# Kernel optimization log

Hardware: AMD Instinct MI355X
Metric: run time of the kernel (lower is better)

## Reference

```python
import jax, jax.numpy as jnp
import numpy as np

N = 131072
E = 524288
H = 128
EPS = 1e-5

def _layernorm(h, g, b):
    mu = jnp.mean(h, axis=-1, keepdims=True)
    var = jnp.mean((h - mu) ** 2, axis=-1, keepdims=True)
    return (h - mu) * jax.lax.rsqrt(var + EPS) * g + b

def _node_to_node(x, senders, receivers, valid, num_nodes, params):
    # two-way (symmetrized) message passing: gather + scatter_add, then MLP+LN
    W1, b1, W2, b2, W3, b3, g, beta = params
    tws = jnp.concatenate([senders, receivers])
    twr = jnp.concatenate([receivers, senders])
    msg = x[tws]  # [2E', H] gather
    if valid is not None:
        msg = jnp.where(jnp.concatenate([valid, valid])[:, None], msg, 0.0)
    agg = jax.ops.segment_sum(msg, twr, num_segments=num_nodes)  # scatter_add
    h = jax.nn.gelu(agg @ W1 + b1, approximate=False)
    h = jax.nn.gelu(h @ W2 + b2, approximate=False)
    h = h @ W3 + b3
    return _layernorm(h, g, beta)

def setup_inputs() -> dict:
    key = jax.random.key(0)
    ks = jax.random.split(key, 20)
    s = 0.05
    inp = {
        "x": jax.random.normal(ks[0], (N, H), dtype=jnp.float32),
        "edge_index": jax.random.randint(ks[1], (2, E), 0, N, dtype=jnp.int32),
        "pool_p": jax.random.normal(ks[2], (H,), dtype=jnp.float32),
    }
    names = ["dW1", "db1", "dW2", "db2", "dW3", "db3", "dg", "dbeta",
             "uW1", "ub1", "uW2", "ub2", "uW3", "ub3", "ug", "ubeta"]
    shapes = [(H, H), (H,), (H, H), (H,), (H, H), (H,), (H,), (H,),
              (2 * H, H), (H,), (H, H), (H,), (H, H), (H,), (H,), (H,)]
    for i, (nm, sh) in enumerate(zip(names, shapes)):
        if nm in ("dg", "ug"):
            inp[nm] = jnp.ones(sh, dtype=jnp.float32)
        elif nm in ("dbeta", "ubeta") or nm.startswith(("db", "ub")):
            inp[nm] = jnp.zeros(sh, dtype=jnp.float32)
        else:
            inp[nm] = jax.random.normal(ks[3 + i], sh, dtype=jnp.float32) * s
    return inp

def reference(x, edge_index, pool_p,
              dW1, db1, dW2, db2, dW3, db3, dg, dbeta,
              uW1, ub1, uW2, ub2, uW3, ub3, ug, ubeta):
    senders, receivers = edge_index[0], edge_index[1]
    k = N // 2  # TopKPooling ratio=0.5

    # ---- down: TopKPooling ----
    score = x @ pool_p / jnp.linalg.norm(pool_p)  # [N]
    _, perm = jax.lax.top_k(score, k)             # kept node indices
    x_skip = x
    x_p = x[perm] * jnp.tanh(score[perm])[:, None]  # [k, H]
    mask = jnp.zeros((N,), dtype=bool).at[perm].set(True)
    mapping = jnp.zeros((N,), dtype=jnp.int32).at[perm].set(
        jnp.arange(k, dtype=jnp.int32))
    valid = mask[senders] & mask[receivers]
    ps, pr = mapping[senders], mapping[receivers]

    # down conv on pooled graph
    x_d = _node_to_node(x_p, ps, pr, valid, k,
                        (dW1, db1, dW2, db2, dW3, db3, dg, dbeta))

    # ---- up: unpool (indexed scatter write) + skip concat + up conv ----
    recovered = jnp.zeros_like(x_skip).at[perm].set(x_d)
    x_u = jnp.concatenate([recovered, x_skip], axis=-1)  # [N, 2H]
    out = _node_to_node(x_u, senders, receivers, None, N,
                        (uW1, ub1, uW2, ub2, uW3, ub3, ug, ubeta))
    return out
```

## Files before the change

### kernel.cpp

```cpp
#include <hip/hip_runtime.h>

#define N_NODES 131072
#define N_EDGES 524288
#define K_TOP   65536
#define LN_EPS  1e-5f
#define N_TILES (N_NODES / 64)
#define BCAP    5120u

typedef unsigned int u32;
typedef unsigned short u16;
typedef unsigned long long u64;

typedef __attribute__((ext_vector_type(8))) short bf8;
typedef __attribute__((ext_vector_type(4))) float f4;

#define ST_OFF    0
#define CANON_OFF (64u<<10)
#define PART_OFF  (576u<<10)
#define KEYS_OFF  (1u<<20)
#define TVAL_OFF  (2u<<20)
#define KEPT_OFF  ((2u<<20)+(512u<<10))
#define SBUF_OFF  (3u<<20)
#define ADJ_OFF   (35u<<20)


#define C_DW1 0
#define C_DB1 16384
#define C_DW2 16512
#define C_DB2 32896
#define C_DW3 33024
#define C_DB3 49408
#define C_DG  49536
#define C_DBE 49664
#define C_UW1 49792
#define C_UB1 82560
#define C_UW2 82688
#define C_UB2 99072
#define C_UW3 99200
#define C_UB3 115584
#define C_UG  115712
#define C_UBE 115840
#define C_TOT 115968
#define CT_DW1 115968
#define CT_DW2 132352
#define CT_DW3 148736
#define CT_UW1 165120
#define CT_UW2 197888
#define CT_UW3 214272
#define CT_TOT 230656

__device__ __forceinline__ float bflo(u32 u){ return __uint_as_float(u << 16); }
__device__ __forceinline__ float bfhi(u32 u){ return __uint_as_float(u & 0xFFFF0000u); }
__device__ __forceinline__ float bf2f(u16 v){ return __uint_as_float(((u32)v) << 16); }
__device__ __forceinline__ u32 f2bf(float f){
  u32 u = __float_as_uint(f);
  return (u + 0x7FFFu + ((u >> 16) & 1u)) >> 16;
}
__device__ __forceinline__ float gelu_f(float x){
  return 0.5f * x * (1.0f + erff(x * 0.7071067811865476f));
}
__device__ __forceinline__ float2 f2add(float2 a, float2 b){
  return make_float2(a.x + b.x, a.y + b.y);
}

__device__ __forceinline__ int swz16(int row, int cc){
  return row * 128 + ((cc ^ (row & 15)) * 8);
}

__device__ __forceinline__ bf8 ld_bf16_chunk(const u32* __restrict__ rowp, int s, int quad){
  uint4 v = *(const uint4*)(rowp + s * 16 + quad * 4);
  return __builtin_bit_cast(bf8, v);
}
__device__ __forceinline__ bf8 scale_bf16_chunk(const u32* __restrict__ rowp, int s, int quad, float tv){
  uint4 v = *(const uint4*)(rowp + s * 16 + quad * 4);
  uint4 q;
  q.x = f2bf(bflo(v.x) * tv) | (f2bf(bfhi(v.x) * tv) << 16);
  q.y = f2bf(bflo(v.y) * tv) | (f2bf(bfhi(v.y) * tv) << 16);
  q.z = f2bf(bflo(v.z) * tv) | (f2bf(bfhi(v.z) * tv) << 16);
  q.w = f2bf(bflo(v.w) * tv) | (f2bf(bfhi(v.w) * tv) << 16);
  return __builtin_bit_cast(bf8, q);
}
__device__ __forceinline__ bf8 cvt_f32_chunk(const float* __restrict__ rowp, int s, int quad, float tv){
  const float* p = rowp + s * 32 + quad * 8;
  float4 f0 = *(const float4*)p;
  float4 f1 = *(const float4*)(p + 4);
  uint4 q;
  q.x = f2bf(f0.x * tv) | (f2bf(f0.y * tv) << 16);
  q.y = f2bf(f0.z * tv) | (f2bf(f0.w * tv) << 16);
  q.z = f2bf(f1.x * tv) | (f2bf(f1.y * tv) << 16);
  q.w = f2bf(f1.z * tv) | (f2bf(f1.w * tv) << 16);
  return __builtin_bit_cast(bf8, q);
}

__device__ __forceinline__ void gemm_ab(const u16* ws, const bf8 a[4], int mn, int quad, f4 acc[8]){
  #pragma unroll
  for (int s = 0; s < 4; s++){
    #pragma unroll
    for (int j = 0; j < 8; j++){
      bf8 b = *(const bf8*)&ws[swz16(j * 16 + mn, s * 4 + quad)];
      acc[j] = __builtin_amdgcn_mfma_f32_16x16x32_bf16(a[s], b, acc[j], 0, 0, 0);
    }
  }
}

struct SelState {
  u64 prefix;
  u32 krem, eqcnt;
  int is_f32;
  u32 pad;
  double inv_norm;
  u32 eqlist[4096];
  u64 eqkey[4096];
};

struct P16 { const void* q[16]; };

__device__ __forceinline__ void chain_step(const u32* __restrict__ tots, int q,
                                           u32* sfx, u32* selb, int t,
                                           u64& pref, u32& target){
  sfx[t] = tots[q * 256 + t];
  __syncthreads();
  for (int o = 1; o < 256; o <<= 1){
    u32 x = (t + o < 256) ? sfx[t + o] : 0u;
    __syncthreads();
    sfx[t] += x;
    __syncthreads();
  }
  u32 above = (t == 255) ? 0u : sfx[t + 1];
  if (sfx[t] >= target && above < target){ selb[0] = (u32)t; selb[1] = target - above; }
  __syncthreads();
  pref = (pref << 8) | (u64)selb[0];
  target = selb[1];
  __syncthreads();
}

__global__ void k_detect(const u32* __restrict__ xw, SelState* st){
  int t = threadIdx.x;
  int cnt = 0;
  for (int i = t; i < 4096; i += 256){
    u32 w = xw[(size_t)i * 2048];
    u32 e = (w >> 23) & 0xFFu;
    if (e >= 97u && e <= 135u) cnt++;
  }
  __shared__ int sh[256];
  sh[t] = cnt; __syncthreads();
  for (int o = 128; o > 0; o >>= 1){ if (t < o) sh[t] += sh[t+o]; __syncthreads(); }
  if (t == 0){
    st->is_f32 = (sh[0] >= 3072) ? 1 : 0;
    st->prefix = 0; st->krem = K_TOP; st->eqcnt = 0;
  }
}

__global__ void k_canon(P16 ps, const SelState* __restrict__ st, u16* __restrict__ canon,
                        u32* __restrict__ tots, u32* __restrict__ gcur){
  int i = blockIdx.x * 256 + threadIdx.x;
  if (i < 1024) tots[i] = 0u;
  if (i < 256)  gcur[i] = (u32)i * BCAP;
  if (i >= CT_TOT) return;
  int isf = st->is_f32;
  if (i < C_TOT){
    const int off[17] = {C_DW1,C_DB1,C_DW2,C_DB2,C_DW3,C_DB3,C_DG,C_DBE,
                         C_UW1,C_UB1,C_UW2,C_UB2,C_UW3,C_UB3,C_UG,C_UBE,C_TOT};
    int seg = 0;
    #pragma unroll
    for (int s2 = 0; s2 < 16; s2++) if (i >= off[s2+1]) seg = s2 + 1;
    int j = i - off[seg];
    if (isf) canon[i] = (u16)f2bf(((const float*)ps.q[seg])[j]);
    else     canon[i] = ((const u16*)ps.q[seg])[j];
  } else {
    const int dst[7] = {CT_DW1, CT_DW2, CT_DW3, CT_UW1, CT_UW2, CT_UW3, CT_TOT};
    const int wq[6]  = {0, 2, 4, 8, 10, 12};
    int g = i;
    int seg = 0;
    #pragma unroll
    for (int s2 = 0; s2 < 6; s2++) if (g >= dst[s2+1]) seg = s2 + 1;
    int loc = g - dst[seg];
    int K = (seg == 3) ? 256 : 128;
    int n = loc / K, k = loc % K;
    int src = k * 128 + n;
    if (isf) canon[g] = (u16)f2bf(((const float*)ps.q[wq[seg]])[src]);
    else     canon[g] = ((const u16*)ps.q[wq[seg]])[src];
  }
}

__global__ __launch_bounds__(256) void k_score(const void* __restrict__ xraw, const void* __restrict__ praw,
                        const SelState* __restrict__ st,
                        u64* __restrict__ keys, float* __restrict__ tval){
  int t = threadIdx.x, lane = t & 63, w = t >> 6;
  int n = blockIdx.x * 4 + w;
  double d, ps;
  if (st->is_f32){
    const float* xf = (const float*)xraw + (size_t)n * 128;
    const float* pf = (const float*)praw;
    double p0 = (double)pf[lane], p1 = (double)pf[64 + lane];
    d  = (double)xf[lane] * p0 + (double)xf[64 + lane] * p1;
    ps = p0 * p0 + p1 * p1;
  } else {
    const u32* xw = (const u32*)xraw + (size_t)n * 64;
    const u32* pw = (const u32*)praw;
    u32 xx = xw[lane], pv = pw[lane];
    double p0 = (double)bflo(pv), p1 = (double)bfhi(pv);
    d  = (double)bflo(xx) * p0 + (double)bfhi(xx) * p1;
    ps = p0 * p0 + p1 * p1;
  }
  for (int o = 32; o > 0; o >>= 1){
    d  += __shfl_down(d,  o, 64);
    ps += __shfl_down(ps, o, 64);
  }
  if (lane == 0){
    double sc = d * (1.0 / sqrt(ps));
    u64 u = (u64)__double_as_longlong(sc);
    u64 key = (u & 0x8000000000000000ULL) ? ~u : (u | 0x8000000000000000ULL);
    keys[n] = key;
    tval[n] = tanhf((float)sc);
  }
}

__global__ __launch_bounds__(256) void k_histp(const u64* __restrict__ keys,
                                               u32* __restrict__ tots, int pass){
  __shared__ u32 sfx[256];
  __shared__ u32 selb[2];
  __shared__ u32 h[256];
  int t = threadIdx.x;
  u64 pref = 0;
  u32 target = K_TOP;
  for (int q = 0; q < pass; q++)
    chain_step(tots, q, sfx, selb, t, pref, target);
  h[t] = 0;
  __syncthreads();
  int sh_d = 56 - 8 * pass;
  for (int n = blockIdx.x * 256 + t; n < N_NODES; n += 256 * 256){
    u64 k = keys[n];
    bool m = (pass == 0) ? true : ((k >> (sh_d + 8)) == pref);
    if (m) atomicAdd(&h[(u32)((k >> sh_d) & 255)], 1u);
  }
  __syncthreads();
  if (h[t]) atomicAdd(&tots[pass * 256 + t], h[t]);
}

__global__ __launch_bounds__(256) void k_mark(const u64* __restrict__ keys,
                                              const u32* __restrict__ tots,
                                              SelState* st, u32* __restrict__ kept){
  __shared__ u32 sfx[256];
  __shared__ u32 selb[2];
  int t = threadIdx.x;
  u64 pref = 0;
  u32 target = K_TOP;
  for (int q = 0; q < 4; q++)
    chain_step(tots, q, sfx, selb, t, pref, target);
  u32 T = (u32)pref;
  int n = blockIdx.x * 256 + t;
  u64 k = keys[n];
  u32 t32 = (u32)(k >> 32);
  kept[n] = (t32 > T) ? 1u : 0u;
  if (t32 == T){
    u32 i = atomicAdd(&st->eqcnt, 1u);
    if (i < 4096){ st->eqlist[i] = (u32)n; st->eqkey[i] = k; }
  }
}

__global__ __launch_bounds__(256) void k_tie(const u32* __restrict__ tots,
                                             SelState* st, u32* __restrict__ kept){
  __shared__ u32 sfx[256];
  __shared__ u32 selb[2];
  int t = threadIdx.x;
  u64 pref = 0;
  u32 target = K_TOP;
  for (int q = 0; q < 4; q++)
    chain_step(tots, q, sfx, selb, t, pref, target);
  u32 r = target;
  u32 m = st->eqcnt; if (m > 4096) m = 4096;
  for (u32 i = t; i < m; i += 256){
    u64 ki = st->eqkey[i]; u32 ii = st->eqlist[i];
    u32 rank = 0;
    for (u32 j = 0; j < m; j++){
      u64 kj = st->eqkey[j];
      rank += (kj > ki || (kj == ki && st->eqlist[j] < ii)) ? 1u : 0u;
    }
    if (rank < r) kept[ii] = 1u;
  }
}

__global__ __launch_bounds__(256) void k_bin(const int* __restrict__ se, const int* __restrict__ re,
                                             u32* __restrict__ gcur, u32* __restrict__ pairs){
  __shared__ u32 cnt[256], sc[256], base[256], cur[256], gpos[256];
  __shared__ u32 stage[8192];
  int t = threadIdx.x;
  cnt[t] = 0;
  __syncthreads();
  int e0 = blockIdx.x * 4096;
  for (int i = t; i < 4096; i += 256){
    int s = se[e0 + i], r = re[e0 + i];
    atomicAdd(&cnt[(u32)r >> 9], 1u);
    atomicAdd(&cnt[(u32)s >> 9], 1u);
  }
  __syncthreads();
  sc[t] = cnt[t];
  __syncthreads();
  for (int o = 1; o < 256; o <<= 1){
    u32 x = (t >= o) ? sc[t - o] : 0u;
    __syncthreads();
    sc[t] += x;
    __syncthreads();
  }
  base[t] = sc[t] - cnt[t];
  cur[t] = base[t];
  gpos[t] = atomicAdd(&gcur[t], cnt[t]);
  __syncthreads();
  for (int i = t; i < 4096; i += 256){
    u32 s = (u32)se[e0 + i], r = (u32)re[e0 + i];
    u32 b1 = r >> 9, p1 = ((r & 511u) << 17) | s;
    u32 b2 = s >> 9, p2 = ((s & 511u) << 17) | r;
    stage[atomicAdd(&cur[b1], 1u)] = p1;
    stage[atomicAdd(&cur[b2], 1u)] = p2;
  }
  __syncthreads();
  int lane = t & 63, wv = t >> 6;
  for (int b = wv; b < 256; b += 4){
    u32 n = cnt[b], src = base[b], dst = gpos[b];
    for (u32 i = lane; i < n; i += 64)
      pairs[dst + i] = stage[src + i];
  }
}

__global__ __launch_bounds__(256) void k_place(const u32* __restrict__ gcur,
                                               const u32* __restrict__ pairs,
                                               u32* __restrict__ adj,
                                               u32* __restrict__ off, u32* __restrict__ end){
  __shared__ u32 cnt[512], cur[512], lo[512], ex2[256];
  int b = blockIdx.x, t = threadIdx.x;
  u32 base = (u32)b * BCAP;
  u32 total = gcur[b] - base;
  cnt[t] = 0; cnt[t + 256] = 0; cur[t] = 0; cur[t + 256] = 0;
  __syncthreads();
  for (u32 i = t; i < total; i += 256)
    atomicAdd(&cnt[pairs[base + i] >> 17], 1u);
  __syncthreads();
  u32 c0 = cnt[2 * t], c1 = cnt[2 * t + 1];
  ex2[t] = c0 + c1;
  __syncthreads();
  for (int o = 1; o < 256; o <<= 1){
    u32 x = (t >= o) ? ex2[t - o] : 0u;
    __syncthreads();
    ex2[t] += x;
    __syncthreads();
  }
  u32 e0 = ex2[t] - c0 - c1;
  int n0 = b * 512 + 2 * t;
  off[n0]     = base + e0;        end[n0]     = base + e0 + c0;
  off[n0 + 1] = base + e0 + c0;   end[n0 + 1] = base + e0 + c0 + c1;
  lo[2 * t] = e0; lo[2 * t + 1] = e0 + c0;
  __syncthreads();
  for (u32 i = t; i < total; i += 256){
    u32 p = pairs[base + i];
    u32 nl = p >> 17;
    u32 slot = base + lo[nl] + atomicAdd(&cur[nl], 1u);
    adj[slot] = p & 0x1FFFFu;
  }
}


__global__ __launch_bounds__(256, 3) void k_proj_down(
    const void* __restrict__ xraw, const float* __restrict__ tval,
    const u16* __restrict__ W1T, const SelState* __restrict__ st,
    const u32* __restrict__ kept, u32* __restrict__ S)
{
  __shared__ u16 w1s[128 * 128];
  __shared__ u16 os[64 * 128];
  int t = threadIdx.x, lane = t & 63, wv = t >> 6;
  int m0 = wv * 16, mn = lane & 15, quad = lane >> 4;

  for (int i = t; i < 2048; i += 256){
    int row = i >> 4, cc = i & 15;
    *(uint4*)&w1s[swz16(row, cc)] = *(const uint4*)(W1T + row * 128 + cc * 8);
  }
  int isf = st->is_f32;
  __syncthreads();

  for (int tile = blockIdx.x; tile < N_TILES; tile += gridDim.x){
    int row0 = tile * 64;
    int arow = row0 + m0 + mn;
    float tv = tval[arow];
    bf8 a[4];
    if (isf){
      const float* xf = (const float*)xraw + (size_t)arow * 128;
      #pragma unroll
      for (int s = 0; s < 4; s++) a[s] = cvt_f32_chunk(xf, s, quad, tv);
    } else {
      const u32* xw = (const u32*)xraw + (size_t)arow * 64;
      #pragma unroll
      for (int s = 0; s < 4; s++) a[s] = scale_bf16_chunk(xw, s, quad, tv);
    }
    f4 acc[8];
    #pragma unroll
    for (int j = 0; j < 8; j++){ acc[j][0]=0.f; acc[j][1]=0.f; acc[j][2]=0.f; acc[j][3]=0.f; }
    gemm_ab(w1s, a, mn, quad, acc);

    #pragma unroll
    for (int j = 0; j < 8; j++){
      int c = j * 16 + mn;
      #pragma unroll
      for (int rg = 0; rg < 4; rg++){
        int row = m0 + quad * 4 + rg;
        os[row * 128 + ((c >> 3) ^ (row & 15)) * 8 + (c & 7)] = (u16)f2bf(acc[j][rg]);
      }
    }
    __builtin_amdgcn_wave_barrier();
    int rl = m0 + (lane >> 2), qt = lane & 3;
    u32 kp = kept[row0 + rl];
    u32* out = S + (size_t)(row0 + rl) * 64;
    #pragma unroll
    for (int i = 0; i < 4; i++){
      int cc = qt * 4 + i;
      uint4 w = *(const uint4*)&os[swz16(rl, cc)];
      if (!kp){ w.x = 0; w.y = 0; w.z = 0; w.w = 0; }
      *(uint4*)(out + cc * 4) = w;
    }
    __builtin_amdgcn_wave_barrier();
  }
}

__global__ __launch_bounds__(256, 2) void k_proj_up(
    const u32* __restrict__ R, const void* __restrict__ xraw,
    const u16* __restrict__ W1T, const SelState* __restrict__ st,
    u32* __restrict__ S2)
{
  __shared__ u16 was[128 * 128];
  __shared__ u16 wbs[128 * 128];
  __shared__ u16 os[64 * 128];
  int t = threadIdx.x, lane = t & 63, wv = t >> 6;
  int m0 = wv * 16, mn = lane & 15, quad = lane >> 4;

  for (int i = t; i < 2048; i += 256){
    int row = i >> 4, cc = i & 15;
    *(uint4*)&was[swz16(row, cc)] = *(const uint4*)(W1T + row * 256 + cc * 8);
    *(uint4*)&wbs[swz16(row, cc)] = *(const uint4*)(W1T + row * 256 + 128 + cc * 8);
  }
  int isf = st->is_f32;
  __syncthreads();

  for (int tile = blockIdx.x; tile < N_TILES; tile += gridDim.x){
    int row0 = tile * 64;
    int arow = row0 + m0 + mn;
    bf8 a[4];
    const u32* rp = R + (size_t)arow * 64;
    #pragma unroll
    for (int s = 0; s < 4; s++) a[s] = ld_bf16_chunk(rp, s, quad);
    f4 acc[8];
    #pragma unroll
    for (int j = 0; j < 8; j++){ acc[j][0]=0.f; acc[j][1]=0.f; acc[j][2]=0.f; acc[j][3]=0.f; }
    gemm_ab(was, a, mn, quad, acc);

    if (isf){
      const float* xf = (const float*)xraw + (size_t)arow * 128;
      #pragma unroll
      for (int s = 0; s < 4; s++) a[s] = cvt_f32_chunk(xf, s, quad, 1.0f);
    } else {
      const u32* xw = (const u32*)xraw + (size_t)arow * 64;
      #pragma unroll
      for (int s = 0; s < 4; s++) a[s] = ld_bf16_chunk(xw, s, quad);
    }
    gemm_ab(wbs, a, mn, quad, acc);

    #pragma unroll
    for (int j = 0; j < 8; j++){
      int c = j * 16 + mn;
      #pragma unroll
      for (int rg = 0; rg < 4; rg++){
        int row = m0 + quad * 4 + rg;
        os[row * 128 + ((c >> 3) ^ (row & 15)) * 8 + (c & 7)] = (u16)f2bf(acc[j][rg]);
      }
    }
    __builtin_amdgcn_wave_barrier();
    int rl = m0 + (lane >> 2), qt = lane & 3;
    u32* out = S2 + (size_t)(row0 + rl) * 64;
    #pragma unroll
    for (int i = 0; i < 4; i++){
      int cc = qt * 4 + i;
      *(uint4*)(out + cc * 4) = *(const uint4*)&os[swz16(rl, cc)];
    }
    __builtin_amdgcn_wave_barrier();
  }
}

template<int IS_DOWN>
__global__ __launch_bounds__(256, 4) void k_agg(
    const u32* __restrict__ Smsg, const u32* __restrict__ off, const u32* __restrict__ end,
    const u32* __restrict__ adj,
    const u16* __restrict__ cb1, const u32* __restrict__ kept,
    u32* __restrict__ H)
{
  int t = threadIdx.x, lane = t & 63, wv = t >> 6;
  float b1l = bf2f(cb1[2 * lane]), b1h = bf2f(cb1[2 * lane + 1]);
  int base = blockIdx.x * 16 + wv * 4;
  #pragma unroll 1
  for (int rr = 0; rr < 4; rr++){
    int n = base + rr;
    if (IS_DOWN && !kept[n]){ H[(size_t)n * 64 + lane] = 0u; continue; }
    u32 jb = off[n], je = end[n];
    float2 a = make_float2(0.f, 0.f);
    u32 j = jb;
    for (; j + 8 <= je; j += 8){
      u32 e0 = adj[j],   e1 = adj[j+1], e2 = adj[j+2], e3 = adj[j+3];
      u32 e4 = adj[j+4], e5 = adj[j+5], e6 = adj[j+6], e7 = adj[j+7];
      u32 w0 = Smsg[(size_t)e0 * 64 + lane];
      u32 w1 = Smsg[(size_t)e1 * 64 + lane];
      u32 w2 = Smsg[(size_t)e2 * 64 + lane];
      u32 w3 = Smsg[(size_t)e3 * 64 + lane];
      u32 w4 = Smsg[(size_t)e4 * 64 + lane];
      u32 w5 = Smsg[(size_t)e5 * 64 + lane];
      u32 w6 = Smsg[(size_t)e6 * 64 + lane];
      u32 w7 = Smsg[(size_t)e7 * 64 + lane];
      float2 v0 = make_float2(bflo(w0), bfhi(w0));
      float2 v1 = make_float2(bflo(w1), bfhi(w1));
      float2 v2 = make_float2(bflo(w2), bfhi(w2));
      float2 v3 = make_float2(bflo(w3), bfhi(w3));
      float2 v4 = make_float2(bflo(w4), bfhi(w4));
      float2 v5 = make_float2(bflo(w5), bfhi(w5));
      float2 v6 = make_float2(bflo(w6), bfhi(w6));
      float2 v7 = make_float2(bflo(w7), bfhi(w7));
      a = f2add(a, f2add(f2add(f2add(v0, v1), f2add(v2, v3)),
                         f2add(f2add(v4, v5), f2add(v6, v7))));
    }
    for (; j + 4 <= je; j += 4){
      u32 e0 = adj[j], e1 = adj[j+1], e2 = adj[j+2], e3 = adj[j+3];
      u32 w0 = Smsg[(size_t)e0 * 64 + lane];
      u32 w1 = Smsg[(size_t)e1 * 64 + lane];
      u32 w2 = Smsg[(size_t)e2 * 64 + lane];
      u32 w3 = Smsg[(size_t)e3 * 64 + lane];
      float2 v0 = make_float2(bflo(w0), bfhi(w0));
      float2 v1 = make_float2(bflo(w1), bfhi(w1));
      float2 v2 = make_float2(bflo(w2), bfhi(w2));
      float2 v3 = make_float2(bflo(w3), bfhi(w3));
      a = f2add(a, f2add(f2add(v0, v1), f2add(v2, v3)));
    }
    for (; j < je; j++){
      u32 w = Smsg[(size_t)adj[j] * 64 + lane];
      a = f2add(a, make_float2(bflo(w), bfhi(w)));
    }
    H[(size_t)n * 64 + lane] = f2bf(gelu_f(a.x + b1l)) | (f2bf(gelu_f(a.y + b1h)) << 16);
  }
}

template<int IS_DOWN>
__global__ __launch_bounds__(256, 2) void k_mlp(
    const u32* __restrict__ H,
    const u16* __restrict__ cW2T, const u16* __restrict__ cb2,
    const u16* __restrict__ cW3T, const u16* __restrict__ cb3,
    const u16* __restrict__ cg, const u16* __restrict__ cbe,
    const u32* __restrict__ kept, const SelState* __restrict__ st,
    u32* __restrict__ Rout, void* __restrict__ fout)
{
  __shared__ u16 w2s[128 * 128];
  __shared__ u16 w3s[128 * 128];
  __shared__ u16 os[64 * 128];
  int t = threadIdx.x, lane = t & 63, wv = t >> 6;
  int m0 = wv * 16, mn = lane & 15, quad = lane >> 4;

  for (int i = t; i < 2048; i += 256){
    int row = i >> 4, cc = i & 15;
    *(uint4*)&w2s[swz16(row, cc)] = *(const uint4*)(cW2T + row * 128 + cc * 8);
    *(uint4*)&w3s[swz16(row, cc)] = *(const uint4*)(cW3T + row * 128 + cc * 8);
  }
  float b2v[8], b3v[8], gv[8], bev[8];
  #pragma unroll
  for (int j = 0; j < 8; j++){
    int c = j * 16 + mn;
    b2v[j] = bf2f(cb2[c]); b3v[j] = bf2f(cb3[c]);
    gv[j]  = bf2f(cg[c]);  bev[j] = bf2f(cbe[c]);
  }
  int isf = st->is_f32;
  __syncthreads();

  for (int tile = blockIdx.x; tile < N_TILES; tile += gridDim.x){
    int row0 = tile * 64;
    int arow = row0 + m0 + mn;

    bf8 a[4];
    const u32* hp = H + (size_t)arow * 64;
    #pragma unroll
    for (int s = 0; s < 4; s++) a[s] = ld_bf16_chunk(hp, s, quad);
    f4 acc[8];
    #pragma unroll
    for (int j = 0; j < 8; j++){ acc[j][0]=0.f; acc[j][1]=0.f; acc[j][2]=0.f; acc[j][3]=0.f; }
    gemm_ab(w2s, a, mn, quad, acc);

    #pragma unroll
    for (int j = 0; j < 8; j++){
      int c = j * 16 + mn;
      #pragma unroll
      for (int rg = 0; rg < 4; rg++){
        int row = m0 + quad * 4 + rg;
        os[row * 128 + ((c >> 3) ^ (row & 15)) * 8 + (c & 7)] = (u16)f2bf(gelu_f(acc[j][rg] + b2v[j]));
      }
    }
    __builtin_amdgcn_wave_barrier();

    #pragma unroll
    for (int s = 0; s < 4; s++) a[s] = *(const bf8*)&os[swz16(m0 + mn, s * 4 + quad)];
    #pragma unroll
    for (int j = 0; j < 8; j++){ acc[j][0]=0.f; acc[j][1]=0.f; acc[j][2]=0.f; acc[j][3]=0.f; }
    gemm_ab(w3s, a, mn, quad, acc);

    #pragma unroll
    for (int j = 0; j < 8; j++){
      #pragma unroll
      for (int rg = 0; rg < 4; rg++) acc[j][rg] += b3v[j];
    }
    float s1[4] = {0.f,0.f,0.f,0.f}, s2[4] = {0.f,0.f,0.f,0.f};
    #pragma unroll
    for (int j = 0; j < 8; j++){
      #pragma unroll
      for (int rg = 0; rg < 4; rg++){
        float v = acc[j][rg];
        s1[rg] += v; s2[rg] += v * v;
      }
    }
    #pragma unroll
    for (int o = 1; o < 16; o <<= 1){
      #pragma unroll
      for (int rg = 0; rg < 4; rg++){
        s1[rg] += __shfl_xor(s1[rg], o, 64);
        s2[rg] += __shfl_xor(s2[rg], o, 64);
      }
    }
    float mu[4], rs[4];
    #pragma unroll
    for (int rg = 0; rg < 4; rg++){
      mu[rg] = s1[rg] * 0.0078125f;
      float var = s2[rg] * 0.0078125f - mu[rg] * mu[rg];
      rs[rg] = rsqrtf(var + LN_EPS);
    }
    #pragma unroll
    for (int j = 0; j < 8; j++){
      #pragma unroll
      for (int rg = 0; rg < 4; rg++)
        acc[j][rg] = (acc[j][rg] - mu[rg]) * rs[rg] * gv[j] + bev[j];
    }

    if (!IS_DOWN && isf){
      float* fo = (float*)fout;
      #pragma unroll
      for (int j = 0; j < 8; j++){
        #pragma unroll
        for (int rg = 0; rg < 4; rg++)
          fo[(size_t)(row0 + m0 + quad * 4 + rg) * 128 + j * 16 + mn] = acc[j][rg];
      }
      continue;
    }

    __builtin_amdgcn_wave_barrier();
    #pragma unroll
    for (int j = 0; j < 8; j++){
      int c = j * 16 + mn;
      #pragma unroll
      for (int rg = 0; rg < 4; rg++){
        int row = m0 + quad * 4 + rg;
        os[row * 128 + ((c >> 3) ^ (row & 15)) * 8 + (c & 7)] = (u16)f2bf(acc[j][rg]);
      }
    }
    __builtin_amdgcn_wave_barrier();
    int rl = m0 + (lane >> 2), qt = lane & 3;
    u32 kp = IS_DOWN ? kept[row0 + rl] : 1u;
    u32* out = (IS_DOWN ? Rout : (u32*)fout) + (size_t)(row0 + rl) * 64;
    #pragma unroll
    for (int i = 0; i < 4; i++){
      int cc = qt * 4 + i;
      uint4 w = *(const uint4*)&os[swz16(rl, cc)];
      if (!kp){ w.x = 0; w.y = 0; w.z = 0; w.w = 0; }
      *(uint4*)(out + cc * 4) = w;
    }
    __builtin_amdgcn_wave_barrier();
  }
}


extern "C" void kernel_launch(void* const* d_in, const int* in_sizes, int n_in,
                              void* d_out, int out_size, void* d_ws, size_t ws_size,
                              hipStream_t stream)
{
  const void* x     = d_in[0];
  const int* eidx   = (const int*)d_in[1];
  const void* poolp = d_in[2];
  const int* senders = eidx;
  const int* receivers = eidx + N_EDGES;

  char* ws = (char*)d_ws;
  SelState* st = (SelState*)(ws + ST_OFF);
  u16*  canon  = (u16*) (ws + CANON_OFF);
  u32*  tots   = (u32*) (ws + PART_OFF);
  u32*  gcur   = (u32*) (ws + PART_OFF + 4096);
  u64*  keys   = (u64*) (ws + KEYS_OFF);
  u32*  off    = (u32*) (ws + KEYS_OFF);
  u32*  end    = (u32*) (ws + KEYS_OFF + (512u<<10));
  float* tval  = (float*)(ws + TVAL_OFF);
  u32*  kept   = (u32*) (ws + KEPT_OFF);
  u32*  Sbuf   = (u32*) (ws + SBUF_OFF);
  u32*  adj    = (u32*) (ws + ADJ_OFF);
  u32*  pairs  = Sbuf;
  u32*  Dbuf   = (u32*) d_out;

  P16 ps;
  for (int i = 0; i < 16; i++) ps.q[i] = d_in[3 + i];

  k_detect<<<1, 256, 0, stream>>>((const u32*)x, st);
  k_canon<<<(CT_TOT + 255) / 256, 256, 0, stream>>>(ps, st, canon, tots, gcur);
  k_score<<<N_NODES / 4, 256, 0, stream>>>(x, poolp, st, keys, tval);
  for (int pass = 0; pass < 4; pass++)
    k_histp<<<256, 256, 0, stream>>>(keys, tots, pass);
  k_mark<<<N_NODES / 256, 256, 0, stream>>>(keys, tots, st, kept);
  k_tie<<<1, 256, 0, stream>>>(tots, st, kept);

  k_bin<<<N_EDGES / 4096, 256, 0, stream>>>(senders, receivers, gcur, pairs);
  k_place<<<256, 256, 0, stream>>>(gcur, pairs, adj, off, end);

  k_proj_down<<<768, 256, 0, stream>>>(x, tval, canon + CT_DW1, st, kept, Sbuf);
  k_agg<1><<<N_NODES / 16, 256, 0, stream>>>(Sbuf, off, end, adj, canon + C_DB1, kept, Dbuf);
  k_mlp<1><<<512, 256, 0, stream>>>(Dbuf,
      canon + CT_DW2, canon + C_DB2, canon + CT_DW3, canon + C_DB3,
      canon + C_DG, canon + C_DBE, kept, st, Sbuf, nullptr);

  k_proj_up<<<512, 256, 0, stream>>>(Sbuf, x, canon + CT_UW1, st, Dbuf);
  k_agg<0><<<N_NODES / 16, 256, 0, stream>>>(Dbuf, off, end, adj, canon + C_UB1, kept, Sbuf);
  k_mlp<0><<<512, 256, 0, stream>>>(Sbuf,
      canon + CT_UW2, canon + C_UB2, canon + CT_UW3, canon + C_UB3,
      canon + C_UG, canon + C_UBE, kept, st, nullptr, d_out);
}
```

Measured before the change: 449.8 us.

## Partition adjacency by kept neighbours so down aggregation skips dropped nodes

k_place now counts, for each node, how many neighbours are kept and orders each adjacency list with kept neighbours first. It packs the kept count and the total count into one word that replaces the end array. The down-pass aggregation reads only the kept prefix, so it no longer gathers zeroed rows of dropped nodes (about three quarters of neighbours when half the nodes are kept). Because those rows are never read, k_proj_down also stops writing them, which saves memory traffic. The cost is extra kept lookups and atomics in k_place.

```diff
diff --git a/kernel.cpp b/kernel.cpp
--- a/kernel.cpp
+++ b/kernel.cpp
@@ -325,16 +325,24 @@
 
 __global__ __launch_bounds__(256) void k_place(const u32* __restrict__ gcur,
                                                const u32* __restrict__ pairs,
+                                               const u32* __restrict__ kept,
                                                u32* __restrict__ adj,
-                                               u32* __restrict__ off, u32* __restrict__ end){
-  __shared__ u32 cnt[512], cur[512], lo[512], ex2[256];
+                                               u32* __restrict__ off, u32* __restrict__ cnts){
+  __shared__ u32 cnt[512], ck[512], curk[512], curn[512], lo[512], ex2[256];
   int b = blockIdx.x, t = threadIdx.x;
   u32 base = (u32)b * BCAP;
   u32 total = gcur[b] - base;
-  cnt[t] = 0; cnt[t + 256] = 0; cur[t] = 0; cur[t + 256] = 0;
-  __syncthreads();
-  for (u32 i = t; i < total; i += 256)
-    atomicAdd(&cnt[pairs[base + i] >> 17], 1u);
+  cnt[t] = 0; cnt[t + 256] = 0;
+  ck[t] = 0;  ck[t + 256] = 0;
+  curk[t] = 0; curk[t + 256] = 0;
+  curn[t] = 0; curn[t + 256] = 0;
+  __syncthreads();
+  for (u32 i = t; i < total; i += 256){
+    u32 p = pairs[base + i];
+    u32 nl = p >> 17, m = p & 0x1FFFFu;
+    atomicAdd(&cnt[nl], 1u);
+    if (kept[m]) atomicAdd(&ck[nl], 1u);
+  }
   __syncthreads();
   u32 c0 = cnt[2 * t], c1 = cnt[2 * t + 1];
   ex2[t] = c0 + c1;
@@ -347,15 +355,19 @@
   }
   u32 e0 = ex2[t] - c0 - c1;
   int n0 = b * 512 + 2 * t;
-  off[n0]     = base + e0;        end[n0]     = base + e0 + c0;
-  off[n0 + 1] = base + e0 + c0;   end[n0 + 1] = base + e0 + c0 + c1;
+  off[n0]     = base + e0;
+  off[n0 + 1] = base + e0 + c0;
+  cnts[n0]     = (ck[2 * t] << 16) | c0;
+  cnts[n0 + 1] = (ck[2 * t + 1] << 16) | c1;
   lo[2 * t] = e0; lo[2 * t + 1] = e0 + c0;
   __syncthreads();
   for (u32 i = t; i < total; i += 256){
     u32 p = pairs[base + i];
-    u32 nl = p >> 17;
-    u32 slot = base + lo[nl] + atomicAdd(&cur[nl], 1u);
-    adj[slot] = p & 0x1FFFFu;
+    u32 nl = p >> 17, m = p & 0x1FFFFu;
+    u32 slot;
+    if (kept[m]) slot = base + lo[nl] + atomicAdd(&curk[nl], 1u);
+    else         slot = base + lo[nl] + ck[nl] + atomicAdd(&curn[nl], 1u);
+    adj[slot] = m;
   }
 }
 
@@ -409,12 +421,12 @@
     int rl = m0 + (lane >> 2), qt = lane & 3;
     u32 kp = kept[row0 + rl];
     u32* out = S + (size_t)(row0 + rl) * 64;
-    #pragma unroll
-    for (int i = 0; i < 4; i++){
-      int cc = qt * 4 + i;
-      uint4 w = *(const uint4*)&os[swz16(rl, cc)];
-      if (!kp){ w.x = 0; w.y = 0; w.z = 0; w.w = 0; }
-      *(uint4*)(out + cc * 4) = w;
+    if (kp){
+      #pragma unroll
+      for (int i = 0; i < 4; i++){
+        int cc = qt * 4 + i;
+        *(uint4*)(out + cc * 4) = *(const uint4*)&os[swz16(rl, cc)];
+      }
     }
     __builtin_amdgcn_wave_barrier();
   }
@@ -485,7 +497,7 @@
 
 template<int IS_DOWN>
 __global__ __launch_bounds__(256, 4) void k_agg(
-    const u32* __restrict__ Smsg, const u32* __restrict__ off, const u32* __restrict__ end,
+    const u32* __restrict__ Smsg, const u32* __restrict__ off, const u32* __restrict__ cnts,
     const u32* __restrict__ adj,
     const u16* __restrict__ cb1, const u32* __restrict__ kept,
     u32* __restrict__ H)
@@ -497,7 +509,9 @@
   for (int rr = 0; rr < 4; rr++){
     int n = base + rr;
     if (IS_DOWN && !kept[n]){ H[(size_t)n * 64 + lane] = 0u; continue; }
-    u32 jb = off[n], je = end[n];
+    u32 c = cnts[n];
+    u32 jb = off[n];
+    u32 je = jb + (IS_DOWN ? (c >> 16) : (c & 0xFFFFu));
     float2 a = make_float2(0.f, 0.f);
     u32 j = jb;
     for (; j + 8 <= je; j += 8){
@@ -692,7 +706,7 @@
   u32*  gcur   = (u32*) (ws + PART_OFF + 4096);
   u64*  keys   = (u64*) (ws + KEYS_OFF);
   u32*  off    = (u32*) (ws + KEYS_OFF);
-  u32*  end    = (u32*) (ws + KEYS_OFF + (512u<<10));
+  u32*  cnts   = (u32*) (ws + KEYS_OFF + (512u<<10));
   float* tval  = (float*)(ws + TVAL_OFF);
   u32*  kept   = (u32*) (ws + KEPT_OFF);
   u32*  Sbuf   = (u32*) (ws + SBUF_OFF);
@@ -712,16 +726,16 @@
   k_tie<<<1, 256, 0, stream>>>(tots, st, kept);
 
   k_bin<<<N_EDGES / 4096, 256, 0, stream>>>(senders, receivers, gcur, pairs);
-  k_place<<<256, 256, 0, stream>>>(gcur, pairs, adj, off, end);
+  k_place<<<256, 256, 0, stream>>>(gcur, pairs, kept, adj, off, cnts);
 
   k_proj_down<<<768, 256, 0, stream>>>(x, tval, canon + CT_DW1, st, kept, Sbuf);
-  k_agg<1><<<N_NODES / 16, 256, 0, stream>>>(Sbuf, off, end, adj, canon + C_DB1, kept, Dbuf);
+  k_agg<1><<<N_NODES / 16, 256, 0, stream>>>(Sbuf, off, cnts, adj, canon + C_DB1, kept, Dbuf);
   k_mlp<1><<<512, 256, 0, stream>>>(Dbuf,
       canon + CT_DW2, canon + C_DB2, canon + CT_DW3, canon + C_DB3,
       canon + C_DG, canon + C_DBE, kept, st, Sbuf, nullptr);
 
   k_proj_up<<<512, 256, 0, stream>>>(Sbuf, x, canon + CT_UW1, st, Dbuf);
-  k_agg<0><<<N_NODES / 16, 256, 0, stream>>>(Dbuf, off, end, adj, canon + C_UB1, kept, Sbuf);
+  k_agg<0><<<N_NODES / 16, 256, 0, stream>>>(Dbuf, off, cnts, adj, canon + C_UB1, kept, Sbuf);
   k_mlp<0><<<512, 256, 0, stream>>>(Sbuf,
       canon + CT_UW2, canon + C_UB2, canon + CT_UW3, canon + C_UB3,
       canon + C_UG, canon + C_UBE, kept, st, nullptr, d_out);
```

After: 441.7 us. About the same (-1.8%).
